# Performance work log

Measured on AMD Instinct MI355X. Metric: run time of the kernel, lower is better.

## Reference

```python
import jax, jax.numpy as jnp
import numpy as np
import math

B, T, D, H, P, NPASS = 2, 2048, 1024, 16, 256, 3


def setup_inputs() -> dict:
    key = jax.random.key(0)
    ks = jax.random.split(key, 8)
    x = jax.random.normal(ks[0], (B, T, D), jnp.float32)
    scale_gamma = 1.0 + 0.1 * jax.random.normal(ks[1], (D,), jnp.float32)
    scale_beta = 0.1 * jax.random.normal(ks[2], (D,), jnp.float32)
    qkv_w = 0.02 * jax.random.normal(ks[3], (3 * D, D), jnp.float32)
    o_w = 0.02 * jax.random.normal(ks[4], (D, D), jnp.float32)
    norm1_w = jnp.ones((D,), jnp.float32)
    norm2_w = jnp.ones((D,), jnp.float32)
    angles = 0.1 * jax.random.normal(ks[5], (NPASS, P), jnp.float32)
    gate = jnp.ones((NPASS, D), jnp.float32)
    bias = jnp.zeros((NPASS, D), jnp.float32)
    # seeded random permutations matching torch.manual_seed(42+p*1000); torch.randperm
    pis, pjs = [], []
    for p in range(NPASS):
        rng = np.random.RandomState(42 + p * 1000)
        perm = rng.permutation(D)
        pis.append(perm[:P])
        pjs.append(perm[P:2 * P])
    pi = jnp.asarray(np.stack(pis), jnp.int32)
    pj = jnp.asarray(np.stack(pjs), jnp.int32)
    return dict(x=x, scale_gamma=scale_gamma, scale_beta=scale_beta, qkv_w=qkv_w,
                o_w=o_w, norm1_w=norm1_w, norm2_w=norm2_w, angles=angles,
                gate=gate, bias=bias, pi=pi, pj=pj)


def _rmsnorm(x, w):
    eps = jnp.finfo(x.dtype).eps
    return x * jax.lax.rsqrt(jnp.mean(x * x, axis=-1, keepdims=True) + eps) * w


def reference(x, scale_gamma, scale_beta, qkv_w, o_w, norm1_w, norm2_w,
              angles, gate, bias, pi, pj):
    Bs, Ts, Ds = x.shape
    hd = Ds // H
    # --- attention branch ---
    h = _rmsnorm(x, norm1_w) * scale_gamma + scale_beta
    qkv = (h @ qkv_w.T).reshape(Bs, Ts, 3, H, hd)
    qkv = jnp.moveaxis(qkv, 2, 0)            # [3, B, T, H, hd]
    q, k, v = (jnp.swapaxes(qkv[i], 1, 2) for i in range(3))  # [B, H, T, hd]
    scores = jnp.einsum('bhqd,bhkd->bhqk', q, k) / math.sqrt(hd)
    causal = jnp.tril(jnp.ones((Ts, Ts), bool))
    scores = jnp.where(causal, scores, -jnp.inf)
    attn = jax.nn.softmax(scores, axis=-1)
    out = jnp.einsum('bhqk,bhkd->bhqd', attn, v)
    out = jnp.swapaxes(out, 1, 2).reshape(Bs, Ts, Ds)
    x = x + out @ o_w.T
    # --- rotation pseudo-FFN branch ---
    h = _rmsnorm(x, norm2_w) * scale_gamma + scale_beta
    r = h
    for p in range(NPASS):
        cos_a = jnp.cos(angles[p])
        sin_a = jnp.sin(angles[p])
        hi = r[..., pi[p]]
        hj = r[..., pj[p]]
        r = r.at[..., pi[p]].set(hi * cos_a - hj * sin_a)
        r = r.at[..., pj[p]].set(hi * sin_a + hj * cos_a)
        r = jax.nn.silu(r * gate[p] + bias[p])
    return x + r - h
```

## Files before the change

### kernel.cpp

```cpp
#include <hip/hip_runtime.h>
#include <hip/hip_bf16.h>

#define B_ 2
#define T_ 2048
#define D_ 1024
#define H_ 16
#define HD_ 64
#define NP_ 3
#define P_ 256

#define SCALE2 0.18033688011112042f

typedef short bf16x8 __attribute__((ext_vector_type(8)));
typedef float f32x4 __attribute__((ext_vector_type(4)));

__device__ __forceinline__ float bf2f(__hip_bfloat16 v) { return __bfloat162float(v); }
__device__ __forceinline__ __hip_bfloat16 f2bf(float v) { return __float2bfloat16(v); }

__device__ __forceinline__ unsigned pack2bf(float a, float b) {
    unsigned r;
    asm("v_cvt_pk_bf16_f32 %0, %1, %2" : "=v"(r) : "v"(a), "v"(b));
    return r;
}
__device__ __forceinline__ unsigned short f2bf_u(float v) {
    return (unsigned short)pack2bf(v, v);
}

#define GLOAD_LDS16(gp, lp) \
    __builtin_amdgcn_global_load_lds( \
        (const __attribute__((address_space(1))) void*)(gp), \
        (__attribute__((address_space(3))) void*)(lp), 16, 0, 0)

__device__ __forceinline__ int block_flag(const unsigned short* xs) {
    __shared__ int fred[4];
    int t = threadIdx.x;
    uint4 v = ((const uint4*)xs)[t];
    int bad = 0;
    unsigned w[4] = {v.x, v.y, v.z, v.w};
#pragma unroll
    for (int i = 0; i < 4; i++) {
        if ((((w[i] & 0xffffu) >> 7) & 0xFF) >= 0xB8) bad++;
        if ((((w[i] >> 16)     >> 7) & 0xFF) >= 0xB8) bad++;
    }
#pragma unroll
    for (int m = 32; m; m >>= 1) bad += __shfl_xor(bad, m, 64);
    if ((t & 63) == 0) fred[t >> 6] = bad;
    __syncthreads();
    return (fred[0] + fred[1] + fred[2] + fred[3]) >= 8;
}

__global__ __launch_bounds__(256) void prep_kernel(
    const void* __restrict__ xraw,
    const void* __restrict__ qkvw, const void* __restrict__ ow,
    const void* __restrict__ g,  const void* __restrict__ b,
    const void* __restrict__ n1, const void* __restrict__ n2,
    const void* __restrict__ ang, const void* __restrict__ gt,
    const void* __restrict__ bi,
    int* __restrict__ flagp,
    __hip_bfloat16* __restrict__ wbf, __hip_bfloat16* __restrict__ owbf,
    float* __restrict__ smalls, __hip_bfloat16* __restrict__ out)
{
    int bid = blockIdx.x;
    int t = threadIdx.x;
    int f = block_flag((const unsigned short*)xraw);
    if (bid == 0 && t == 0) *flagp = f;

    if (bid < 2048) {
        const int na = 3 * D_ * D_;
        int i8 = (bid * 256 + t) * 8;
        const void* src; __hip_bfloat16* dst; int off;
        if (i8 < na) { src = qkvw; dst = wbf; off = i8; }
        else         { src = ow;   dst = owbf; off = i8 - na; }
        if (f) {
            const float4* sp = (const float4*)((const float*)src + off);
            float4 v0 = sp[0], v1 = sp[1];
            uint4 o;
            o.x = pack2bf(v0.x, v0.y);
            o.y = pack2bf(v0.z, v0.w);
            o.z = pack2bf(v1.x, v1.y);
            o.w = pack2bf(v1.z, v1.w);
            *(uint4*)(dst + off) = o;
        } else {
            *(uint4*)(dst + off) = *(const uint4*)((const __hip_bfloat16*)src + off);
        }
        return;
    }
    if (bid < 6144) {
        int row = bid - 2048;
        float eps = f ? 1.1920929e-7f : 0.0078125f;
        float v[4], ga[4], be[4], ww[4];
        if (f) {
            const float4 xv = ((const float4*)((const float*)xraw + (size_t)row * D_))[t];
            v[0] = xv.x; v[1] = xv.y; v[2] = xv.z; v[3] = xv.w;
            const float4 gv = ((const float4*)g)[t];
            ga[0] = gv.x; ga[1] = gv.y; ga[2] = gv.z; ga[3] = gv.w;
            const float4 bv = ((const float4*)b)[t];
            be[0] = bv.x; be[1] = bv.y; be[2] = bv.z; be[3] = bv.w;
            const float4 wv4 = ((const float4*)n1)[t];
            ww[0] = wv4.x; ww[1] = wv4.y; ww[2] = wv4.z; ww[3] = wv4.w;
        } else {
            const uint2 u = ((const uint2*)((const __hip_bfloat16*)xraw + (size_t)row * D_))[t];
            v[0] = __uint_as_float(u.x << 16);
            v[1] = __uint_as_float(u.x & 0xffff0000u);
            v[2] = __uint_as_float(u.y << 16);
            v[3] = __uint_as_float(u.y & 0xffff0000u);
#pragma unroll
            for (int c = 0; c < 4; c++) {
                int e = t * 4 + c;
                ga[c] = bf2f(((const __hip_bfloat16*)g)[e]);
                be[c] = bf2f(((const __hip_bfloat16*)b)[e]);
                ww[c] = bf2f(((const __hip_bfloat16*)n1)[e]);
            }
        }
        float ss = 0.f;
#pragma unroll
        for (int c = 0; c < 4; c++) ss += v[c] * v[c];
#pragma unroll
        for (int m = 32; m; m >>= 1) ss += __shfl_xor(ss, m, 64);
        __shared__ float red[4];
        int wv = t >> 6;
        if ((t & 63) == 0) red[wv] = ss;
        __syncthreads();
        float scale = rsqrtf((red[0] + red[1] + red[2] + red[3]) * (1.0f / D_) + eps);
        float o[4];
#pragma unroll
        for (int c = 0; c < 4; c++)
            o[c] = v[c] * scale * ww[c] * ga[c] + be[c];
        uint2 pkd;
        pkd.x = pack2bf(o[0], o[1]);
        pkd.y = pack2bf(o[2], o[3]);
        *(uint2*)(out + (size_t)row * D_ + t * 4) = pkd;
        return;
    }
    {
        int i = (bid - 6144) * 256 + t;
        if (i >= 11008) return;
        const void* src; int off;
        if      (i < 1024) { src = g;   off = i; }
        else if (i < 2048) { src = b;   off = i - 1024; }
        else if (i < 3072) { src = n1;  off = i - 2048; }
        else if (i < 4096) { src = n2;  off = i - 3072; }
        else if (i < 4864) { src = ang; off = i - 4096; }
        else if (i < 7936) { src = gt;  off = i - 4864; }
        else               { src = bi;  off = i - 7936; }
        smalls[i] = f ? ((const float*)src)[off]
                      : bf2f(((const __hip_bfloat16*)src)[off]);
    }
}

__global__ __launch_bounds__(256) void gemm_bt_bf16_kernel(
    const __hip_bfloat16* __restrict__ A,
    const __hip_bfloat16* __restrict__ Bm,
    __hip_bfloat16* __restrict__ C,
    int M, int N, int K, int nscale, float qscale)
{
    __shared__ __attribute__((aligned(16))) __hip_bfloat16 As[128 * 64];
    __shared__ __attribute__((aligned(16))) __hip_bfloat16 Bs[128 * 64];
    int tid = threadIdx.x;
    int bm = blockIdx.y, bn = blockIdx.x;
    int lane = tid & 63, wv = tid >> 6;
    int wm = wv >> 1, wn = wv & 1;
    int q = lane >> 4, mr = lane & 15;
    int m8 = mr & 7;

    f32x4 acc[4][4] = {};

    for (int k0 = 0; k0 < K; k0 += 64) {
#pragma unroll
        for (int s = 0; s < 4; s++) {
            int e = (s * 256 + tid) * 8;
            int r = e >> 6;
            int pc = (e >> 3) & 7;
            int gc = (pc ^ (r & 7)) * 8;
            GLOAD_LDS16(&A[(size_t)(bm * 128 + r) * K + k0 + gc], &As[e]);
            GLOAD_LDS16(&Bm[(size_t)(bn * 128 + r) * K + k0 + gc], &Bs[e]);
        }
        __syncthreads();
#pragma unroll
        for (int h = 0; h < 2; h++) {
            bf16x8 af[4], bfr[4];
#pragma unroll
            for (int i = 0; i < 4; i++)
                af[i] = *(const bf16x8*)(&As[(wm * 64 + i * 16 + mr) * 64 + (((h * 4 + q) ^ m8) * 8)]);
#pragma unroll
            for (int j = 0; j < 4; j++)
                bfr[j] = *(const bf16x8*)(&Bs[(wn * 64 + j * 16 + mr) * 64 + (((h * 4 + q) ^ m8) * 8)]);
#pragma unroll
            for (int i = 0; i < 4; i++)
#pragma unroll
                for (int j = 0; j < 4; j++)
                    acc[i][j] = __builtin_amdgcn_mfma_f32_16x16x32_bf16(af[i], bfr[j], acc[i][j], 0, 0, 0);
        }
        __syncthreads();
    }

#pragma unroll
    for (int i = 0; i < 4; i++)
#pragma unroll
        for (int r = 0; r < 4; r++) {
            int m = bm * 128 + wm * 64 + i * 16 + q * 4 + r;
#pragma unroll
            for (int j = 0; j < 4; j++) {
                int n = bn * 128 + wn * 64 + j * 16 + mr;
                float vv = acc[i][j][r];
                if (n < nscale) vv *= qscale;
                ((unsigned short*)C)[(size_t)m * N + n] = f2bf_u(vv);
            }
        }
}

__global__ __launch_bounds__(256) void gemm_o64_resid_kernel(
    const __hip_bfloat16* __restrict__ A,
    const __hip_bfloat16* __restrict__ Bm,
    const void* __restrict__ xraw,
    const int* __restrict__ flag,
    float* __restrict__ C,
    int M, int N, int K)
{
    __shared__ __attribute__((aligned(16))) __hip_bfloat16 As[128 * 64];
    __shared__ __attribute__((aligned(16))) __hip_bfloat16 Bs[64 * 64];
    int tid = threadIdx.x;
    int bn = blockIdx.x, bm = blockIdx.y;
    int lane = tid & 63, wv = tid >> 6;
    int q = lane >> 4, mr = lane & 15;
    int m8 = mr & 7;
    int f = *flag;

    f32x4 acc[2][4] = {};

    for (int k0 = 0; k0 < K; k0 += 64) {
#pragma unroll
        for (int s = 0; s < 4; s++) {
            int e = (s * 256 + tid) * 8;
            int r = e >> 6;
            int pc = (e >> 3) & 7;
            int gc = (pc ^ (r & 7)) * 8;
            GLOAD_LDS16(&A[(size_t)(bm * 128 + r) * K + k0 + gc], &As[e]);
        }
#pragma unroll
        for (int s = 0; s < 2; s++) {
            int e = (s * 256 + tid) * 8;
            int r = e >> 6;
            int pc = (e >> 3) & 7;
            int gc = (pc ^ (r & 7)) * 8;
            GLOAD_LDS16(&Bm[(size_t)(bn * 64 + r) * K + k0 + gc], &Bs[e]);
        }
        __syncthreads();
#pragma unroll
        for (int h = 0; h < 2; h++) {
            bf16x8 af[2], bfr[4];
#pragma unroll
            for (int i = 0; i < 2; i++)
                af[i] = *(const bf16x8*)(&As[(wv * 32 + i * 16 + mr) * 64 + (((h * 4 + q) ^ m8) * 8)]);
#pragma unroll
            for (int j = 0; j < 4; j++)
                bfr[j] = *(const bf16x8*)(&Bs[(j * 16 + mr) * 64 + (((h * 4 + q) ^ m8) * 8)]);
#pragma unroll
            for (int i = 0; i < 2; i++)
#pragma unroll
                for (int j = 0; j < 4; j++)
                    acc[i][j] = __builtin_amdgcn_mfma_f32_16x16x32_bf16(af[i], bfr[j], acc[i][j], 0, 0, 0);
        }
        __syncthreads();
    }

#pragma unroll
    for (int i = 0; i < 2; i++)
#pragma unroll
        for (int r = 0; r < 4; r++) {
            int m = bm * 128 + wv * 32 + i * 16 + q * 4 + r;
#pragma unroll
            for (int j = 0; j < 4; j++) {
                int n = bn * 64 + j * 16 + mr;
                size_t idx = (size_t)m * N + n;
                float rv = f ? ((const float*)xraw)[idx]
                             : bf2f(((const __hip_bfloat16*)xraw)[idx]);
                C[idx] = rv + acc[i][j][r];
            }
        }
}

__global__ __launch_bounds__(256, 4) void attn_kernel(
    const __hip_bfloat16* __restrict__ qkv,
    __hip_bfloat16* __restrict__ attn_out)
{
    __shared__ __attribute__((aligned(16))) __hip_bfloat16 Ks[2][64 * 64];
    __shared__ __attribute__((aligned(16))) __hip_bfloat16 Vts[2][64 * 64];
    __shared__ __attribute__((aligned(16))) unsigned int Pd[4 * 512];

    int id = blockIdx.x;
    int half = (id ^ (id >> 8)) & 1;
    int w4 = (id >> 1) & 15;
    int qt = half ? 31 - w4 : w4;
    int bh = (id >> 5) & 31;
    int b = bh >> 4, h = bh & 15;
    int tid = threadIdx.x, lane = tid & 63, wv = tid >> 6;
    int q = lane >> 4, mr = lane & 15;
    int m8 = mr & 7;

    const size_t rs3 = 3 * D_;
    const __hip_bfloat16* qp = qkv + (size_t)(b * T_) * rs3 + h * HD_;
    const __hip_bfloat16* kp = qp + D_;
    const __hip_bfloat16* vp = qp + 2 * D_;

    int sr = tid >> 2;
    int sc = (tid & 3) * 16;
    int lc0 = sc >> 3;
    int swk = sr & 7;
    int kk_ = (tid & 31) * 2;
    int dd = (tid >> 5) * 8;
    int vlc = kk_ >> 3, voff = kk_ & 7;

    bf16x8 aq0, aq1;
    {
        const __hip_bfloat16* qrow = qp + (size_t)(qt * 64 + wv * 16 + mr) * rs3;
        aq0 = *(const bf16x8*)(qrow + q * 8);
        aq1 = *(const bf16x8*)(qrow + 32 + q * 8);
    }

    bf16x8 kr0 = *(const bf16x8*)(kp + (size_t)sr * rs3 + sc);
    bf16x8 kr1 = *(const bf16x8*)(kp + (size_t)sr * rs3 + sc + 8);
    bf16x8 vr0 = *(const bf16x8*)(vp + (size_t)kk_ * rs3 + dd);
    bf16x8 vr1 = *(const bf16x8*)(vp + (size_t)(kk_ + 1) * rs3 + dd);
    *(bf16x8*)(&Ks[0][sr * 64 + ((lc0 ^ swk) * 8)]) = kr0;
    *(bf16x8*)(&Ks[0][sr * 64 + (((lc0 + 1) ^ swk) * 8)]) = kr1;
    {
        unsigned int* vd = (unsigned int*)&Vts[0][0];
        union { bf16x8 v; unsigned u[4]; } ua, ub;
        ua.v = vr0; ub.v = vr1;
#pragma unroll
        for (int w = 0; w < 4; w++) {
            unsigned lo = __builtin_amdgcn_perm(ub.u[w], ua.u[w], 0x05040100u);
            unsigned hi = __builtin_amdgcn_perm(ub.u[w], ua.u[w], 0x07060302u);
            int i0 = 2 * w, i1 = 2 * w + 1;
            vd[((dd + i0) * 64 + ((vlc ^ i0) * 8 + voff)) >> 1] = lo;
            vd[((dd + i1) * 64 + ((vlc ^ i1) * 8 + voff)) >> 1] = hi;
        }
    }
    __syncthreads();

    float l_part = 0.f;
    f32x4 o_acc[4] = {};
    unsigned int* Pw = &Pd[wv * 512];
    int qloc = wv * 16 + mr;

    for (int s = 0; s <= qt; s++) {
        int buf = s & 1;

        if (s < qt) {
            int ktn = s + 1;
            kr0 = *(const bf16x8*)(kp + (size_t)(ktn * 64 + sr) * rs3 + sc);
            kr1 = *(const bf16x8*)(kp + (size_t)(ktn * 64 + sr) * rs3 + sc + 8);
            vr0 = *(const bf16x8*)(vp + (size_t)(ktn * 64 + kk_) * rs3 + dd);
            vr1 = *(const bf16x8*)(vp + (size_t)(ktn * 64 + kk_ + 1) * rs3 + dd);
        }

        f32x4 sv[4] = {};
        {
            const __hip_bfloat16* Kb = &Ks[buf][0];
            __builtin_amdgcn_s_setprio(1);
#pragma unroll
            for (int jn = 0; jn < 4; jn++)
                sv[jn] = __builtin_amdgcn_mfma_f32_16x16x32_bf16(
                    *(const bf16x8*)(&Kb[(jn * 16 + mr) * 64 + ((q ^ m8) * 8)]),
                    aq0, sv[jn], 0, 0, 0);
#pragma unroll
            for (int jn = 0; jn < 4; jn++)
                sv[jn] = __builtin_amdgcn_mfma_f32_16x16x32_bf16(
                    *(const bf16x8*)(&Kb[(jn * 16 + mr) * 64 + (((4 + q) ^ m8) * 8)]),
                    aq1, sv[jn], 0, 0, 0);
            __builtin_amdgcn_s_setprio(0);
        }

        if (s == qt) {
#pragma unroll
            for (int jn = 0; jn < 4; jn++)
#pragma unroll
                for (int r = 0; r < 4; r++)
                    if (jn * 16 + q * 4 + r > qloc) sv[jn][r] = -1e30f;
        }

#pragma unroll
        for (int jn = 0; jn < 4; jn++)
#pragma unroll
            for (int r = 0; r < 4; r++) {
                float p = exp2f(sv[jn][r]);
                sv[jn][r] = p;
                l_part += p;
            }

#pragma unroll
        for (int jn = 0; jn < 4; jn++) {
            uint2 val;
            val.x = pack2bf(sv[jn][0], sv[jn][1]);
            val.y = pack2bf(sv[jn][2], sv[jn][3]);
            int dw4 = 2 * jn + (q >> 1);
            *(uint2*)(&Pw[mr * 32 + ((dw4 ^ m8) << 2) + 2 * (q & 1)]) = val;
        }

        __builtin_amdgcn_s_setprio(1);
#pragma unroll
        for (int kk = 0; kk < 2; kk++) {
            bf16x8 bp = *(const bf16x8*)(&Pw[mr * 32 + (((4 * kk + q) ^ m8) << 2)]);
#pragma unroll
            for (int dt = 0; dt < 4; dt++) {
                bf16x8 bv = *(const bf16x8*)(&Vts[buf][(dt * 16 + mr) * 64 + (((kk * 4 + q) ^ m8) * 8)]);
                o_acc[dt] = __builtin_amdgcn_mfma_f32_16x16x32_bf16(bv, bp, o_acc[dt], 0, 0, 0);
            }
        }
        __builtin_amdgcn_s_setprio(0);

        if (s < qt) {
            *(bf16x8*)(&Ks[buf ^ 1][sr * 64 + ((lc0 ^ swk) * 8)]) = kr0;
            *(bf16x8*)(&Ks[buf ^ 1][sr * 64 + (((lc0 + 1) ^ swk) * 8)]) = kr1;
            unsigned int* vd = (unsigned int*)&Vts[buf ^ 1][0];
            union { bf16x8 v; unsigned u[4]; } ua, ub;
            ua.v = vr0; ub.v = vr1;
#pragma unroll
            for (int w = 0; w < 4; w++) {
                unsigned lo = __builtin_amdgcn_perm(ub.u[w], ua.u[w], 0x05040100u);
                unsigned hi = __builtin_amdgcn_perm(ub.u[w], ua.u[w], 0x07060302u);
                int i0 = 2 * w, i1 = 2 * w + 1;
                vd[((dd + i0) * 64 + ((vlc ^ i0) * 8 + voff)) >> 1] = lo;
                vd[((dd + i1) * 64 + ((vlc ^ i1) * 8 + voff)) >> 1] = hi;
            }
        }
        __syncthreads();
    }

    float l_run = l_part;
    l_run += __shfl_xor(l_run, 16, 64);
    l_run += __shfl_xor(l_run, 32, 64);

    {
        float inv = 1.0f / l_run;
        int trow = qt * 64 + wv * 16 + mr;
        __hip_bfloat16* op = attn_out + (size_t)(b * T_ + trow) * D_ + h * HD_;
#pragma unroll
        for (int dt = 0; dt < 4; dt++) {
            uint2 val;
            val.x = pack2bf(o_acc[dt][0] * inv, o_acc[dt][1] * inv);
            val.y = pack2bf(o_acc[dt][2] * inv, o_acc[dt][3] * inv);
            *(uint2*)(op + dt * 16 + q * 4) = val;
        }
    }
}

__global__ __launch_bounds__(256) void final_kernel(
    const float* __restrict__ xn,
    const float* __restrict__ gamma,
    const float* __restrict__ beta,
    const float* __restrict__ w2,
    const float* __restrict__ angles,
    const float* __restrict__ gate,
    const float* __restrict__ bias,
    const int* __restrict__ pi,
    const int* __restrict__ pj,
    const int* __restrict__ flag,
    void* __restrict__ outp)
{
    __shared__ float rbuf[D_];
    __shared__ float red[4];
    int row = blockIdx.x, t = threadIdx.x;
    int f = *flag;
    float eps = f ? 1.1920929e-7f : 0.0078125f;
    const float4 xv = ((const float4*)(xn + (size_t)row * D_))[t];
    float x4[4] = {xv.x, xv.y, xv.z, xv.w};
    float ss = 0.f;
#pragma unroll
    for (int c = 0; c < 4; c++) ss += x4[c] * x4[c];
#pragma unroll
    for (int m = 32; m; m >>= 1) ss += __shfl_xor(ss, m, 64);
    int wv = t >> 6;
    if ((t & 63) == 0) red[wv] = ss;
    __syncthreads();
    float scale = rsqrtf((red[0] + red[1] + red[2] + red[3]) * (1.0f / D_) + eps);
    float hloc[4];
#pragma unroll
    for (int c = 0; c < 4; c++) {
        int e = t * 4 + c;
        float hv = x4[c] * scale * w2[e] * gamma[e] + beta[e];
        hloc[c] = hv;
        rbuf[e] = hv;
    }
    __syncthreads();
    for (int p = 0; p < NP_; p++) {
        float a = angles[p * P_ + t];
        float ca = __cosf(a), sa = __sinf(a);
        int ip = pi[p * P_ + t], jp = pj[p * P_ + t];
        float hi = rbuf[ip], hj = rbuf[jp];
        rbuf[ip] = hi * ca - hj * sa;
        rbuf[jp] = hi * sa + hj * ca;
        __syncthreads();
#pragma unroll
        for (int c = 0; c < 4; c++) {
            int e = t * 4 + c;
            float v = rbuf[e] * gate[p * D_ + e] + bias[p * D_ + e];
            rbuf[e] = v / (1.f + __expf(-v));
        }
        __syncthreads();
    }
#pragma unroll
    for (int c = 0; c < 4; c++) {
        int e = t * 4 + c;
        float ov = x4[c] + rbuf[e] - hloc[c];
        size_t idx = (size_t)row * D_ + e;
        if (f) ((float*)outp)[idx] = ov;
        else   ((__hip_bfloat16*)outp)[idx] = f2bf(ov);
    }
}

extern "C" void kernel_launch(void* const* d_in, const int* in_sizes, int n_in,
                              void* d_out, int out_size, void* d_ws, size_t ws_size,
                              hipStream_t stream)
{
    const void* x      = d_in[0];
    const void* gamma  = d_in[1];
    const void* beta   = d_in[2];
    const void* qkv_w  = d_in[3];
    const void* o_w    = d_in[4];
    const void* n1w    = d_in[5];
    const void* n2w    = d_in[6];
    const void* angles = d_in[7];
    const void* gate   = d_in[8];
    const void* bias   = d_in[9];
    const int* pi = (const int*)d_in[10];
    const int* pj = (const int*)d_in[11];

    const int M = B_ * T_;
    char* ws = (char*)d_ws;
    const size_t MB = 1u << 20;
    int*   flag   = (int*)ws;
    float* smalls = (float*)(ws + 4096);
    float* gf   = smalls;
    float* bf   = smalls + 1024;
    float* n2f  = smalls + 3072;
    float* angf = smalls + 4096;
    float* gtf  = smalls + 4864;
    float* bif  = smalls + 7936;
    __hip_bfloat16* wbf  = (__hip_bfloat16*)(ws + 17 * MB);
    __hip_bfloat16* owbf = (__hip_bfloat16*)(ws + 23 * MB);
    __hip_bfloat16* h1   = (__hip_bfloat16*)(ws + 25 * MB);
    __hip_bfloat16* qkv  = (__hip_bfloat16*)(ws + 33 * MB);
    float*          xnew = (float*)         (ws + 33 * MB);

    prep_kernel<<<6187, 256, 0, stream>>>(
        x, qkv_w, o_w, gamma, beta, n1w, n2w, angles, gate, bias,
        flag, wbf, owbf, smalls, h1);

    gemm_bt_bf16_kernel<<<dim3(3 * D_ / 128, M / 128), 256, 0, stream>>>(
        h1, wbf, qkv, M, 3 * D_, D_, D_, SCALE2);

    attn_kernel<<<dim3(1024), 256, 0, stream>>>(qkv, h1);

    gemm_o64_resid_kernel<<<dim3(D_ / 64, M / 128), 256, 0, stream>>>(
        h1, owbf, x, flag, xnew, M, D_, D_);

    final_kernel<<<M, 256, 0, stream>>>(xnew, gf, bf, n2f, angf, gtf, bif,
                                        pi, pj, flag, d_out);
}
```

Measured before the change: 213.6 us.

## Process one row per wavefront in final kernel to remove block barriers

The final RMSNorm and rotation kernel now gives each 64-lane wavefront a whole row, with four rows per block and a private LDS buffer per wave. The row-sum reduction and the rotation and SiLU passes no longer need block-wide __syncthreads. Gate, bias, angle and index loads are widened to float4/int4. It relies on the lanes of one wavefront seeing each other's LDS writes in program order without a barrier, and each lane now keeps more registers live per row.

Result: no change. 217.4 us (+1.8%).

```diff
diff --git a/kernel.cpp b/kernel.cpp
--- a/kernel.cpp
+++ b/kernel.cpp
@@ -459,54 +459,85 @@
     const int* __restrict__ flag,
     void* __restrict__ outp)
 {
-    __shared__ float rbuf[D_];
-    __shared__ float red[4];
-    int row = blockIdx.x, t = threadIdx.x;
+    __shared__ float rbuf4[4][D_];
+    int t = threadIdx.x;
+    int lane = t & 63, wvi = t >> 6;
+    int row = blockIdx.x * 4 + wvi;
+    float* rbuf = rbuf4[wvi];
     int f = *flag;
     float eps = f ? 1.1920929e-7f : 0.0078125f;
-    const float4 xv = ((const float4*)(xn + (size_t)row * D_))[t];
-    float x4[4] = {xv.x, xv.y, xv.z, xv.w};
+    const float* xr = xn + (size_t)row * D_;
+
+    float x4[16], hloc[16];
     float ss = 0.f;
 #pragma unroll
-    for (int c = 0; c < 4; c++) ss += x4[c] * x4[c];
+    for (int g = 0; g < 4; g++) {
+        float4 xv = *(const float4*)(xr + g * 256 + lane * 4);
+        x4[g * 4 + 0] = xv.x; x4[g * 4 + 1] = xv.y;
+        x4[g * 4 + 2] = xv.z; x4[g * 4 + 3] = xv.w;
+        ss += xv.x * xv.x + xv.y * xv.y + xv.z * xv.z + xv.w * xv.w;
+    }
 #pragma unroll
     for (int m = 32; m; m >>= 1) ss += __shfl_xor(ss, m, 64);
-    int wv = t >> 6;
-    if ((t & 63) == 0) red[wv] = ss;
-    __syncthreads();
-    float scale = rsqrtf((red[0] + red[1] + red[2] + red[3]) * (1.0f / D_) + eps);
-    float hloc[4];
-#pragma unroll
-    for (int c = 0; c < 4; c++) {
-        int e = t * 4 + c;
-        float hv = x4[c] * scale * w2[e] * gamma[e] + beta[e];
-        hloc[c] = hv;
-        rbuf[e] = hv;
-    }
-    __syncthreads();
+    float scale = rsqrtf(ss * (1.0f / D_) + eps);
+#pragma unroll
+    for (int g = 0; g < 4; g++) {
+        float4 wv4 = *(const float4*)(w2 + g * 256 + lane * 4);
+        float4 gv = *(const float4*)(gamma + g * 256 + lane * 4);
+        float4 bv = *(const float4*)(beta + g * 256 + lane * 4);
+        float wq[4] = {wv4.x, wv4.y, wv4.z, wv4.w};
+        float gq[4] = {gv.x, gv.y, gv.z, gv.w};
+        float bq[4] = {bv.x, bv.y, bv.z, bv.w};
+#pragma unroll
+        for (int c = 0; c < 4; c++) {
+            int e = g * 256 + lane * 4 + c;
+            float hv = x4[g * 4 + c] * scale * wq[c] * gq[c] + bq[c];
+            hloc[g * 4 + c] = hv;
+            rbuf[e] = hv;
+        }
+    }
+
     for (int p = 0; p < NP_; p++) {
-        float a = angles[p * P_ + t];
-        float ca = __cosf(a), sa = __sinf(a);
-        int ip = pi[p * P_ + t], jp = pj[p * P_ + t];
-        float hi = rbuf[ip], hj = rbuf[jp];
-        rbuf[ip] = hi * ca - hj * sa;
-        rbuf[jp] = hi * sa + hj * ca;
-        __syncthreads();
+        float4 av = *(const float4*)(angles + p * P_ + lane * 4);
+        int4 ipv = *(const int4*)(pi + p * P_ + lane * 4);
+        int4 jpv = *(const int4*)(pj + p * P_ + lane * 4);
+        float aa[4] = {av.x, av.y, av.z, av.w};
+        int ip4[4] = {ipv.x, ipv.y, ipv.z, ipv.w};
+        int jp4[4] = {jpv.x, jpv.y, jpv.z, jpv.w};
+        float hi4[4], hj4[4];
+#pragma unroll
+        for (int i = 0; i < 4; i++) { hi4[i] = rbuf[ip4[i]]; hj4[i] = rbuf[jp4[i]]; }
+#pragma unroll
+        for (int i = 0; i < 4; i++) {
+            float ca = __cosf(aa[i]), sa = __sinf(aa[i]);
+            rbuf[ip4[i]] = hi4[i] * ca - hj4[i] * sa;
+            rbuf[jp4[i]] = hi4[i] * sa + hj4[i] * ca;
+        }
+#pragma unroll
+        for (int g = 0; g < 4; g++) {
+            float4 gv = *(const float4*)(gate + p * D_ + g * 256 + lane * 4);
+            float4 bv = *(const float4*)(bias + p * D_ + g * 256 + lane * 4);
+            float gq[4] = {gv.x, gv.y, gv.z, gv.w};
+            float bq[4] = {bv.x, bv.y, bv.z, bv.w};
+#pragma unroll
+            for (int c = 0; c < 4; c++) {
+                int e = g * 256 + lane * 4 + c;
+                float v = rbuf[e] * gq[c] + bq[c];
+                rbuf[e] = v / (1.f + __expf(-v));
+            }
+        }
+    }
+
+#pragma unroll
+    for (int g = 0; g < 4; g++) {
 #pragma unroll
         for (int c = 0; c < 4; c++) {
-            int e = t * 4 + c;
-            float v = rbuf[e] * gate[p * D_ + e] + bias[p * D_ + e];
-            rbuf[e] = v / (1.f + __expf(-v));
-        }
-        __syncthreads();
-    }
-#pragma unroll
-    for (int c = 0; c < 4; c++) {
-        int e = t * 4 + c;
-        float ov = x4[c] + rbuf[e] - hloc[c];
-        size_t idx = (size_t)row * D_ + e;
-        if (f) ((float*)outp)[idx] = ov;
-        else   ((__hip_bfloat16*)outp)[idx] = f2bf(ov);
+            int e = g * 256 + lane * 4 + c;
+            float ov = x4[g * 4 + c] + rbuf[e] - hloc[g * 4 + c];
+            size_t idx = (size_t)row * D_ + e;
+            if (f) ((float*)outp)[idx] = ov;
+            else   ((__hip_bfloat16*)outp)[idx] = f2bf(ov);
+        }
     }
 }
 
@@ -556,6 +587,6 @@
     gemm_o64_resid_kernel<<<dim3(D_ / 64, M / 128), 256, 0, stream>>>(
         h1, owbf, x, flag, xnew, M, D_, D_);
 
-    final_kernel<<<M, 256, 0, stream>>>(xnew, gf, bf, n2f, angf, gtf, bif,
-                                        pi, pj, flag, d_out);
-}
+    final_kernel<<<M / 4, 256, 0, stream>>>(xnew, gf, bf, n2f, angf, gtf, bif,
+                                            pi, pj, flag, d_out);
+}
```
